# Optimization experiments

Hardware: AMD Instinct MI355X
Metric: run time of the kernel (lower is better)

Reference implementation:

```python
import jax, jax.numpy as jnp
import numpy as np

FEATURE_DIM = 128

def setup_inputs() -> dict:
    key0 = jax.random.key(0)
    k1, k2, k3 = jax.random.split(key0, 3)
    B, NQ, NK, D = 4, 4096, 4096, FEATURE_DIM
    return {
        "target": jax.random.normal(k1, (B, NQ, D), dtype=jnp.float32),
        "key": jax.random.normal(k2, (B, NK, D), dtype=jnp.float32),
        "value": jax.random.normal(k3, (B, NK, D), dtype=jnp.float32),
    }

def reference(target, key, value):
    # Lan_K F: scores = target @ key^T / sqrt(d); weights = softmax(scores); out = weights @ value
    scale = 1.0 / np.sqrt(FEATURE_DIM).astype(np.float32)
    scores = jnp.einsum('bqd,bkd->bqk', target, key) * scale  # [B, NQ, NK]
    weights = jax.nn.softmax(scores, axis=-1)
    return jnp.einsum('bqk,bkd->bqd', weights, value)  # [B, NQ, D]
```

## Files before the change

### kernel.cpp

```cpp
#include <hip/hip_runtime.h>
#include <stdint.h>

#define B_ 4
#define NQ_ 4096
#define NK_ 4096
#define D_ 128
#define BM_ 64
#define BN_ 128
#define NITER_ (NK_/BN_)
#define PS_ 136
#define OS_ 66

typedef __attribute__((ext_vector_type(8))) short short8;
typedef __attribute__((ext_vector_type(4))) float floatx4;
typedef unsigned int u32;

union frag_u { u32 u[4]; short8 s; };
union pair_u { u32 u[2]; uint2 v; };

__device__ __forceinline__ unsigned short f2bf_rne(float x){
  union { float f; u32 u; } c; c.f = x;
  u32 u = c.u;
  return (unsigned short)((u + 0x7fffu + ((u >> 16) & 1u)) >> 16);
}
__device__ __forceinline__ u32 pk2bf(float a, float b){
  union { float f; u32 u; } x, y; x.f = a; y.f = b;
  return ((x.u + 0x8000u) >> 16) | ((y.u + 0x8000u) & 0xffff0000u);
}

__global__ __launch_bounds__(256) void prep_kernel(
    const float* __restrict__ k, const float* __restrict__ v,
    unsigned short* __restrict__ kf, unsigned short* __restrict__ vf){
  __shared__ __align__(16) char smem[40960];
  const int t = threadIdx.x;
  const int blk = blockIdx.x;
  if (blk < 128){
    int b = blk >> 5, it = blk & 31;
    const float* src = k + ((size_t)b*NK_ + it*BN_)*D_;
    #pragma unroll
    for (int i = 0; i < 16; i++){
      int f = t + i*256;
      int row = f >> 5, c4 = f & 31;
      float4 a = *(const float4*)(src + (size_t)row*D_ + c4*4);
      ushort4 s;
      s.x = f2bf_rne(a.x); s.y = f2bf_rne(a.y);
      s.z = f2bf_rne(a.z); s.w = f2bf_rne(a.w);
      int kg = row >> 5, rem = row & 31;
      int dh = (rem >> 2) & 1;
      int l15 = ((rem >> 3) << 2) | (rem & 3);
      int wq = kg*2 + dh;
      int j = c4 >> 3, l4 = (c4 >> 1) & 3, half = c4 & 1;
      *(ushort4*)(smem + (wq*4 + j)*1088 + l4*272 + l15*16 + half*8) = s;
    }
    __syncthreads();
    unsigned short* dst = kf + (size_t)(b*32 + it)*2048*8;
    #pragma unroll
    for (int i = 0; i < 8; i++){
      int c = t + i*256;
      int lane = c & 63, j = (c >> 6) & 3, wq = c >> 8;
      int l15 = lane & 15, l4 = lane >> 4;
      short8 x = *(const short8*)(smem + (wq*4 + j)*1088 + l4*272 + l15*16);
      *(short8*)(dst + (size_t)c*8) = x;
    }
  } else {
    int blk2 = blk - 128;
    int b = blk2 >> 5, it = blk2 & 31;
    const float* src = v + ((size_t)b*NK_ + it*BN_)*D_;
    #pragma unroll
    for (int i = 0; i < 16; i++){
      int f = t + i*256;
      int row = f >> 5, c4 = f & 31;
      float4 a = *(const float4*)(src + (size_t)row*D_ + c4*4);
      float vals[4] = {a.x, a.y, a.z, a.w};
      int kk = row & 7, l4a = (row >> 3) & 3, kga = row >> 5;
      #pragma unroll
      for (int jj = 0; jj < 4; jj++){
        int d = c4*4 + jj;
        int dh = d >> 6, dt = (d >> 4) & 3, l15 = d & 15;
        int c = ((kga*2 + dh)*4 + dt)*64 + l4a*16 + l15;
        *(unsigned short*)(smem + c*16 + (c>>2)*16 + kk*2) = f2bf_rne(vals[jj]);
      }
    }
    __syncthreads();
    unsigned short* dst = vf + (size_t)(b*32 + it)*2048*8;
    #pragma unroll
    for (int i = 0; i < 8; i++){
      int c = t + i*256;
      short8 x = *(const short8*)(smem + c*16 + (c>>2)*16);
      *(short8*)(dst + (size_t)c*8) = x;
    }
  }
}

__global__ __launch_bounds__(512, 2) void attn_kernel(
    const float* __restrict__ Qf, const unsigned short* __restrict__ Kb,
    const unsigned short* __restrict__ Vt, float* __restrict__ Out){
  __shared__ __align__(16) char sm[69632];
  unsigned short* smP = (unsigned short*)sm;
  float* smO = (float*)sm;
  float* smL = (float*)(sm + 67584);

  const int bi = blockIdx.x;
  const int b  = (bi >> 1) & 3;
  const int qt = ((bi >> 3) << 1) | (bi & 1);
  const int q0 = qt * BM_;
  const int tid = threadIdx.x;
  const int w = tid >> 6, lane = tid & 63;
  const int kg = w >> 1, dh = w & 1;
  const int l15 = lane & 15, l4 = lane >> 4;

  const short8* Kfrag = (const short8*)Kb;
  const short8* Vfrag = (const short8*)Vt;
  const size_t FSTRIDE = 8*4*64;
  const size_t fbase = (((size_t)b*32)*8 + w)*4*64 + lane;

  short8 qf[4][4];
  {
    const float* qp = Qf + ((size_t)b*NQ_ + q0)*D_;
    #pragma unroll
    for (int nb = 0; nb < 4; nb++)
      #pragma unroll
      for (int kb = 0; kb < 4; kb++){
        const float* p = qp + (size_t)(nb*16 + l15)*D_ + kb*32 + l4*8;
        float4 a = *(const float4*)p;
        float4 c4 = *(const float4*)(p + 4);
        frag_u f;
        f.u[0] = pk2bf(a.x, a.y);  f.u[1] = pk2bf(a.z, a.w);
        f.u[2] = pk2bf(c4.x, c4.y); f.u[3] = pk2bf(c4.z, c4.w);
        qf[nb][kb] = f.s;
      }
  }

  short8 kfA[4], kfB[4], vfA[4], vfB[4];
  #pragma unroll
  for (int j = 0; j < 4; j++) kfA[j] = Kfrag[fbase + j*64];
  #pragma unroll
  for (int dt = 0; dt < 4; dt++) vfA[dt] = Vfrag[fbase + dt*64];
  #pragma unroll
  for (int j = 0; j < 4; j++) kfB[j] = Kfrag[fbase + FSTRIDE + j*64];
  #pragma unroll
  for (int dt = 0; dt < 4; dt++) vfB[dt] = Vfrag[fbase + FSTRIDE + dt*64];

  floatx4 o[4][4];
  #pragma unroll
  for (int nb = 0; nb < 4; nb++)
    #pragma unroll
    for (int dt = 0; dt < 4; dt++) o[nb][dt] = (floatx4)0.0f;
  float lsum[4] = {0.f, 0.f, 0.f, 0.f};

  const float SL = 0.08838834764831845f * 1.4426950408889634f;
  const size_t prow = (size_t)kg*32 + l4*8;

  for (int it = 0; it < NITER_; it += 2){
    {
      floatx4 s[4];
      #pragma unroll
      for (int nb = 0; nb < 4; nb++){
        s[nb] = (floatx4)0.0f;
        s[nb] = __builtin_amdgcn_mfma_f32_16x16x32_bf16(kfA[0], qf[nb][0], s[nb], 0,0,0);
        s[nb] = __builtin_amdgcn_mfma_f32_16x16x32_bf16(kfA[1], qf[nb][1], s[nb], 0,0,0);
        s[nb] = __builtin_amdgcn_mfma_f32_16x16x32_bf16(kfA[2], qf[nb][2], s[nb], 0,0,0);
        s[nb] = __builtin_amdgcn_mfma_f32_16x16x32_bf16(kfA[3], qf[nb][3], s[nb], 0,0,0);
      }
      if (it + 2 < NITER_){
        #pragma unroll
        for (int j = 0; j < 4; j++)
          kfA[j] = Kfrag[fbase + (size_t)(it+2)*FSTRIDE + j*64];
      }
      unsigned short* smPb = smP;
      #pragma unroll
      for (int nb = 0; nb < 4; nb++){
        float p0 = __builtin_amdgcn_exp2f(s[nb][0] * SL);
        float p1 = __builtin_amdgcn_exp2f(s[nb][1] * SL);
        float p2 = __builtin_amdgcn_exp2f(s[nb][2] * SL);
        float p3 = __builtin_amdgcn_exp2f(s[nb][3] * SL);
        lsum[nb] += (p0 + p1) + (p2 + p3);
        pair_u pp; pp.u[0] = pk2bf(p0, p1); pp.u[1] = pk2bf(p2, p3);
        *(uint2*)(smPb + (size_t)(nb*16 + l15)*PS_ + prow + dh*4) = pp.v;
      }
      asm volatile("s_waitcnt lgkmcnt(0)" ::: "memory");
      __builtin_amdgcn_s_barrier();
      asm volatile("" ::: "memory");
      short8 pf[4];
      #pragma unroll
      for (int nb = 0; nb < 4; nb++)
        pf[nb] = *(const short8*)(smPb + (size_t)(nb*16 + l15)*PS_ + prow);
      #pragma unroll
      for (int nb = 0; nb < 4; nb++)
        #pragma unroll
        for (int dt = 0; dt < 4; dt++)
          o[nb][dt] = __builtin_amdgcn_mfma_f32_16x16x32_bf16(pf[nb], vfA[dt], o[nb][dt], 0,0,0);
      if (it + 2 < NITER_){
        #pragma unroll
        for (int dt = 0; dt < 4; dt++)
          vfA[dt] = Vfrag[fbase + (size_t)(it+2)*FSTRIDE + dt*64];
      }
    }
    {
      floatx4 s[4];
      #pragma unroll
      for (int nb = 0; nb < 4; nb++){
        s[nb] = (floatx4)0.0f;
        s[nb] = __builtin_amdgcn_mfma_f32_16x16x32_bf16(kfB[0], qf[nb][0], s[nb], 0,0,0);
        s[nb] = __builtin_amdgcn_mfma_f32_16x16x32_bf16(kfB[1], qf[nb][1], s[nb], 0,0,0);
        s[nb] = __builtin_amdgcn_mfma_f32_16x16x32_bf16(kfB[2], qf[nb][2], s[nb], 0,0,0);
        s[nb] = __builtin_amdgcn_mfma_f32_16x16x32_bf16(kfB[3], qf[nb][3], s[nb], 0,0,0);
      }
      if (it + 3 < NITER_){
        #pragma unroll
        for (int j = 0; j < 4; j++)
          kfB[j] = Kfrag[fbase + (size_t)(it+3)*FSTRIDE + j*64];
      }
      unsigned short* smPb = smP + 64*PS_;
      #pragma unroll
      for (int nb = 0; nb < 4; nb++){
        float p0 = __builtin_amdgcn_exp2f(s[nb][0] * SL);
        float p1 = __builtin_amdgcn_exp2f(s[nb][1] * SL);
        float p2 = __builtin_amdgcn_exp2f(s[nb][2] * SL);
        float p3 = __builtin_amdgcn_exp2f(s[nb][3] * SL);
        lsum[nb] += (p0 + p1) + (p2 + p3);
        pair_u pp; pp.u[0] = pk2bf(p0, p1); pp.u[1] = pk2bf(p2, p3);
        *(uint2*)(smPb + (size_t)(nb*16 + l15)*PS_ + prow + dh*4) = pp.v;
      }
      asm volatile("s_waitcnt lgkmcnt(0)" ::: "memory");
      __builtin_amdgcn_s_barrier();
      asm volatile("" ::: "memory");
      short8 pf[4];
      #pragma unroll
      for (int nb = 0; nb < 4; nb++)
        pf[nb] = *(const short8*)(smPb + (size_t)(nb*16 + l15)*PS_ + prow);
      #pragma unroll
      for (int nb = 0; nb < 4; nb++)
        #pragma unroll
        for (int dt = 0; dt < 4; dt++)
          o[nb][dt] = __builtin_amdgcn_mfma_f32_16x16x32_bf16(pf[nb], vfB[dt], o[nb][dt], 0,0,0);
      if (it + 3 < NITER_){
        #pragma unroll
        for (int dt = 0; dt < 4; dt++)
          vfB[dt] = Vfrag[fbase + (size_t)(it+3)*FSTRIDE + dt*64];
      }
    }
  }

  #pragma unroll
  for (int nb = 0; nb < 4; nb++){
    float v = lsum[nb];
    v += __shfl_xor(v, 16);
    v += __shfl_xor(v, 32);
    lsum[nb] = v;
  }
  if (l4 == 0)
    #pragma unroll
    for (int nb = 0; nb < 4; nb++)
      smL[w*64 + nb*16 + l15] = lsum[nb];

  __syncthreads();

  if (w >= 4){
    float* r = smO + (size_t)(w - 4) * 4224;
    #pragma unroll
    for (int nb = 0; nb < 4; nb++)
      #pragma unroll
      for (int dt = 0; dt < 4; dt++)
        #pragma unroll
        for (int q = 0; q < 4; q++)
          r[(size_t)(nb*16 + l4*4 + q)*OS_ + dt*16 + l15] = o[nb][dt][q];
  }
  __syncthreads();
  if (w < 4){
    float* r = smO + (size_t)w * 4224;
    #pragma unroll
    for (int nb = 0; nb < 4; nb++)
      #pragma unroll
      for (int dt = 0; dt < 4; dt++)
        #pragma unroll
        for (int q = 0; q < 4; q++)
          o[nb][dt][q] += r[(size_t)(nb*16 + l4*4 + q)*OS_ + dt*16 + l15];
  }
  __syncthreads();
  if (w == 2 || w == 3){
    float* r = smO + (size_t)(w - 2) * 4224;
    #pragma unroll
    for (int nb = 0; nb < 4; nb++)
      #pragma unroll
      for (int dt = 0; dt < 4; dt++)
        #pragma unroll
        for (int q = 0; q < 4; q++)
          r[(size_t)(nb*16 + l4*4 + q)*OS_ + dt*16 + l15] = o[nb][dt][q];
  }
  __syncthreads();
  if (w < 2){
    float* r = smO + (size_t)w * 4224;
    float* og = Out + ((size_t)b*NQ_ + q0)*D_ + dh*64;
    #pragma unroll
    for (int nb = 0; nb < 4; nb++)
      #pragma unroll
      for (int q = 0; q < 4; q++){
        int row = nb*16 + l4*4 + q;
        float lt = 0.f;
        #pragma unroll
        for (int w2 = 0; w2 < 8; w2++) lt += smL[w2*64 + row];
        float inv = 1.0f / lt;
        #pragma unroll
        for (int dt = 0; dt < 4; dt++){
          float val = o[nb][dt][q] + r[(size_t)row*OS_ + dt*16 + l15];
          og[(size_t)row*D_ + dt*16 + l15] = val * inv;
        }
      }
  }
}

extern "C" void kernel_launch(void* const* d_in, const int* in_sizes, int n_in,
                              void* d_out, int out_size, void* d_ws, size_t ws_size,
                              hipStream_t stream){
  const float* q = (const float*)d_in[0];
  const float* k = (const float*)d_in[1];
  const float* v = (const float*)d_in[2];
  float* out = (float*)d_out;
  unsigned short* kb = (unsigned short*)d_ws;
  unsigned short* vt = kb + (size_t)B_*NK_*D_;
  prep_kernel<<<256, 256, 0, stream>>>(k, v, kb, vt);
  attn_kernel<<<256, 512, 0, stream>>>(q, kb, vt, out);
}
```

Baseline: 117.3 us.

## Fuse K/V prep and attention into one kernel with grid barriers

Merges the bf16 K/V repacking kernel into the attention kernel, separated by a software grid barrier built on a global atomic counter. The repacked K/V now live in the output buffer rather than the workspace, and a second grid barrier keeps every block from writing its output until all blocks have finished reading the fragments. The aim is to remove one kernel launch and the gap between the two kernels. The barrier relies on all 256 blocks being resident at the same time, and the output buffer holds exactly as many bytes as the two bf16 copies, so no space is left over.

```diff
diff --git a/kernel.cpp b/kernel.cpp
--- a/kernel.cpp
+++ b/kernel.cpp
@@ -28,18 +28,38 @@
   return ((x.u + 0x8000u) >> 16) | ((y.u + 0x8000u) & 0xffff0000u);
 }
 
-__global__ __launch_bounds__(256) void prep_kernel(
-    const float* __restrict__ k, const float* __restrict__ v,
-    unsigned short* __restrict__ kf, unsigned short* __restrict__ vf){
-  __shared__ __align__(16) char smem[40960];
-  const int t = threadIdx.x;
-  const int blk = blockIdx.x;
-  if (blk < 128){
-    int b = blk >> 5, it = blk & 31;
-    const float* src = k + ((size_t)b*NK_ + it*BN_)*D_;
-    #pragma unroll
-    for (int i = 0; i < 16; i++){
-      int f = t + i*256;
+__device__ unsigned g_bar = 0;
+__device__ __forceinline__ void grid_barrier(){
+  __threadfence();
+  __syncthreads();
+  if (threadIdx.x == 0){
+    unsigned old = __hip_atomic_fetch_add(&g_bar, 1u, __ATOMIC_ACQ_REL,
+                                          __HIP_MEMORY_SCOPE_AGENT);
+    unsigned target = (old & ~255u) + 256u;
+    while ((int)(__hip_atomic_load(&g_bar, __ATOMIC_ACQUIRE,
+                                   __HIP_MEMORY_SCOPE_AGENT) - target) < 0)
+      __builtin_amdgcn_s_sleep(8);
+  }
+  __syncthreads();
+  __threadfence();
+}
+
+__global__ __launch_bounds__(512, 2) void fused_kernel(
+    const float* __restrict__ Qf, const float* __restrict__ Kin,
+    const float* __restrict__ Vin, float* Out){
+  __shared__ __align__(16) char sm[69632];
+  const int tid = threadIdx.x;
+  const int bi = blockIdx.x;
+
+  unsigned short* kb = (unsigned short*)Out;
+  unsigned short* vt = kb + (size_t)B_*NK_*D_;
+
+  if (bi < 128){
+    int b = bi >> 5, it = bi & 31;
+    const float* src = Kin + ((size_t)b*NK_ + it*BN_)*D_;
+    #pragma unroll
+    for (int i = 0; i < 8; i++){
+      int f = tid + i*512;
       int row = f >> 5, c4 = f & 31;
       float4 a = *(const float4*)(src + (size_t)row*D_ + c4*4);
       ushort4 s;
@@ -50,25 +70,25 @@
       int l15 = ((rem >> 3) << 2) | (rem & 3);
       int wq = kg*2 + dh;
       int j = c4 >> 3, l4 = (c4 >> 1) & 3, half = c4 & 1;
-      *(ushort4*)(smem + (wq*4 + j)*1088 + l4*272 + l15*16 + half*8) = s;
+      *(ushort4*)(sm + (wq*4 + j)*1088 + l4*272 + l15*16 + half*8) = s;
     }
     __syncthreads();
-    unsigned short* dst = kf + (size_t)(b*32 + it)*2048*8;
-    #pragma unroll
-    for (int i = 0; i < 8; i++){
-      int c = t + i*256;
+    unsigned short* dst = kb + (size_t)(b*32 + it)*2048*8;
+    #pragma unroll
+    for (int i = 0; i < 4; i++){
+      int c = tid + i*512;
       int lane = c & 63, j = (c >> 6) & 3, wq = c >> 8;
       int l15 = lane & 15, l4 = lane >> 4;
-      short8 x = *(const short8*)(smem + (wq*4 + j)*1088 + l4*272 + l15*16);
+      short8 x = *(const short8*)(sm + (wq*4 + j)*1088 + l4*272 + l15*16);
       *(short8*)(dst + (size_t)c*8) = x;
     }
   } else {
-    int blk2 = blk - 128;
+    int blk2 = bi - 128;
     int b = blk2 >> 5, it = blk2 & 31;
-    const float* src = v + ((size_t)b*NK_ + it*BN_)*D_;
-    #pragma unroll
-    for (int i = 0; i < 16; i++){
-      int f = t + i*256;
+    const float* src = Vin + ((size_t)b*NK_ + it*BN_)*D_;
+    #pragma unroll
+    for (int i = 0; i < 8; i++){
+      int f = tid + i*512;
       int row = f >> 5, c4 = f & 31;
       float4 a = *(const float4*)(src + (size_t)row*D_ + c4*4);
       float vals[4] = {a.x, a.y, a.z, a.w};
@@ -78,39 +98,34 @@
         int d = c4*4 + jj;
         int dh = d >> 6, dt = (d >> 4) & 3, l15 = d & 15;
         int c = ((kga*2 + dh)*4 + dt)*64 + l4a*16 + l15;
-        *(unsigned short*)(smem + c*16 + (c>>2)*16 + kk*2) = f2bf_rne(vals[jj]);
+        *(unsigned short*)(sm + c*16 + (c>>2)*16 + kk*2) = f2bf_rne(vals[jj]);
       }
     }
     __syncthreads();
-    unsigned short* dst = vf + (size_t)(b*32 + it)*2048*8;
-    #pragma unroll
-    for (int i = 0; i < 8; i++){
-      int c = t + i*256;
-      short8 x = *(const short8*)(smem + c*16 + (c>>2)*16);
+    unsigned short* dst = vt + (size_t)(b*32 + it)*2048*8;
+    #pragma unroll
+    for (int i = 0; i < 4; i++){
+      int c = tid + i*512;
+      short8 x = *(const short8*)(sm + c*16 + (c>>2)*16);
       *(short8*)(dst + (size_t)c*8) = x;
     }
   }
-}
-
-__global__ __launch_bounds__(512, 2) void attn_kernel(
-    const float* __restrict__ Qf, const unsigned short* __restrict__ Kb,
-    const unsigned short* __restrict__ Vt, float* __restrict__ Out){
-  __shared__ __align__(16) char sm[69632];
+
+  grid_barrier();
+
   unsigned short* smP = (unsigned short*)sm;
   float* smO = (float*)sm;
   float* smL = (float*)(sm + 67584);
 
-  const int bi = blockIdx.x;
   const int b  = (bi >> 1) & 3;
   const int qt = ((bi >> 3) << 1) | (bi & 1);
   const int q0 = qt * BM_;
-  const int tid = threadIdx.x;
   const int w = tid >> 6, lane = tid & 63;
   const int kg = w >> 1, dh = w & 1;
   const int l15 = lane & 15, l4 = lane >> 4;
 
-  const short8* Kfrag = (const short8*)Kb;
-  const short8* Vfrag = (const short8*)Vt;
+  const short8* Kfrag = (const short8*)kb;
+  const short8* Vfrag = (const short8*)vt;
   const size_t FSTRIDE = 8*4*64;
   const size_t fbase = (((size_t)b*32)*8 + w)*4*64 + lane;
 
@@ -120,14 +135,14 @@
     #pragma unroll
     for (int nb = 0; nb < 4; nb++)
       #pragma unroll
-      for (int kb = 0; kb < 4; kb++){
-        const float* p = qp + (size_t)(nb*16 + l15)*D_ + kb*32 + l4*8;
+      for (int kbq = 0; kbq < 4; kbq++){
+        const float* p = qp + (size_t)(nb*16 + l15)*D_ + kbq*32 + l4*8;
         float4 a = *(const float4*)p;
         float4 c4 = *(const float4*)(p + 4);
         frag_u f;
         f.u[0] = pk2bf(a.x, a.y);  f.u[1] = pk2bf(a.z, a.w);
         f.u[2] = pk2bf(c4.x, c4.y); f.u[3] = pk2bf(c4.z, c4.w);
-        qf[nb][kb] = f.s;
+        qf[nb][kbq] = f.s;
       }
   }
 
@@ -242,6 +257,8 @@
     }
   }
 
+  grid_barrier();
+
   #pragma unroll
   for (int nb = 0; nb < 4; nb++){
     float v = lsum[nb];
@@ -317,8 +334,6 @@
   const float* k = (const float*)d_in[1];
   const float* v = (const float*)d_in[2];
   float* out = (float*)d_out;
-  unsigned short* kb = (unsigned short*)d_ws;
-  unsigned short* vt = kb + (size_t)B_*NK_*D_;
-  prep_kernel<<<256, 256, 0, stream>>>(k, v, kb, vt);
-  attn_kernel<<<256, 512, 0, stream>>>(q, kb, vt, out);
-}
+  (void)d_ws; (void)ws_size;
+  fused_kernel<<<256, 512, 0, stream>>>(q, k, v, out);
+}
```

After: 291.6 us. 149% more time.

## Compute scores redundantly per wave pair to drop LDS P exchange and barriers

Applied to the files above, without the earlier changes.

Each wave now computes the QK^T scores for the full 32-key slice it consumes in the PV product, using two sets of K fragments. The exponentiated probabilities are packed straight into the MFMA A-operand register fragment instead of going through shared memory. This removes the per-subiteration LDS write/read and the workgroup barrier. In exchange the QK MFMA work is doubled, since both dh waves compute the same scores, and K fragment register pressure grows. The row-sum normalisation is halved (2/lt) because lsum is now counted twice.

```diff
diff --git a/kernel.cpp b/kernel.cpp
--- a/kernel.cpp
+++ b/kernel.cpp
@@ -8,7 +8,6 @@
 #define BM_ 64
 #define BN_ 128
 #define NITER_ (NK_/BN_)
-#define PS_ 136
 #define OS_ 66
 
 typedef __attribute__((ext_vector_type(8))) short short8;
@@ -16,7 +15,6 @@
 typedef unsigned int u32;
 
 union frag_u { u32 u[4]; short8 s; };
-union pair_u { u32 u[2]; uint2 v; };
 
 __device__ __forceinline__ unsigned short f2bf_rne(float x){
   union { float f; u32 u; } c; c.f = x;
@@ -92,11 +90,51 @@
   }
 }
 
+#define SUBITER(KF, VF, ITN) do {                                              \
+  _Pragma("unroll")                                                            \
+  for (int nb = 0; nb < 4; nb++){                                              \
+    floatx4 s0 = (floatx4)0.0f, s1 = (floatx4)0.0f;                            \
+    s0 = __builtin_amdgcn_mfma_f32_16x16x32_bf16(KF[0][0], qf[nb][0], s0,0,0,0);\
+    s0 = __builtin_amdgcn_mfma_f32_16x16x32_bf16(KF[0][1], qf[nb][1], s0,0,0,0);\
+    s0 = __builtin_amdgcn_mfma_f32_16x16x32_bf16(KF[0][2], qf[nb][2], s0,0,0,0);\
+    s0 = __builtin_amdgcn_mfma_f32_16x16x32_bf16(KF[0][3], qf[nb][3], s0,0,0,0);\
+    s1 = __builtin_amdgcn_mfma_f32_16x16x32_bf16(KF[1][0], qf[nb][0], s1,0,0,0);\
+    s1 = __builtin_amdgcn_mfma_f32_16x16x32_bf16(KF[1][1], qf[nb][1], s1,0,0,0);\
+    s1 = __builtin_amdgcn_mfma_f32_16x16x32_bf16(KF[1][2], qf[nb][2], s1,0,0,0);\
+    s1 = __builtin_amdgcn_mfma_f32_16x16x32_bf16(KF[1][3], qf[nb][3], s1,0,0,0);\
+    float p0 = __builtin_amdgcn_exp2f(s0[0] * SL);                             \
+    float p1 = __builtin_amdgcn_exp2f(s0[1] * SL);                             \
+    float p2 = __builtin_amdgcn_exp2f(s0[2] * SL);                             \
+    float p3 = __builtin_amdgcn_exp2f(s0[3] * SL);                             \
+    float p4 = __builtin_amdgcn_exp2f(s1[0] * SL);                             \
+    float p5 = __builtin_amdgcn_exp2f(s1[1] * SL);                             \
+    float p6 = __builtin_amdgcn_exp2f(s1[2] * SL);                             \
+    float p7 = __builtin_amdgcn_exp2f(s1[3] * SL);                             \
+    lsum[nb] += ((p0 + p1) + (p2 + p3)) + ((p4 + p5) + (p6 + p7));             \
+    frag_u pf;                                                                 \
+    pf.u[0] = pk2bf(p0, p1); pf.u[1] = pk2bf(p2, p3);                          \
+    pf.u[2] = pk2bf(p4, p5); pf.u[3] = pk2bf(p6, p7);                          \
+    o[nb][0] = __builtin_amdgcn_mfma_f32_16x16x32_bf16(pf.s, VF[0], o[nb][0],0,0,0);\
+    o[nb][1] = __builtin_amdgcn_mfma_f32_16x16x32_bf16(pf.s, VF[1], o[nb][1],0,0,0);\
+    o[nb][2] = __builtin_amdgcn_mfma_f32_16x16x32_bf16(pf.s, VF[2], o[nb][2],0,0,0);\
+    o[nb][3] = __builtin_amdgcn_mfma_f32_16x16x32_bf16(pf.s, VF[3], o[nb][3],0,0,0);\
+  }                                                                            \
+  if ((ITN) < NITER_){                                                         \
+    _Pragma("unroll")                                                          \
+    for (int h = 0; h < 2; h++)                                                \
+      _Pragma("unroll")                                                        \
+      for (int j = 0; j < 4; j++)                                              \
+        KF[h][j] = Kfrag[kbase[h] + (size_t)(ITN)*FSTRIDE + j*64];             \
+    _Pragma("unroll")                                                          \
+    for (int dt = 0; dt < 4; dt++)                                             \
+      VF[dt] = Vfrag[vbase + (size_t)(ITN)*FSTRIDE + dt*64];                   \
+  }                                                                            \
+} while(0)
+
 __global__ __launch_bounds__(512, 2) void attn_kernel(
     const float* __restrict__ Qf, const unsigned short* __restrict__ Kb,
     const unsigned short* __restrict__ Vt, float* __restrict__ Out){
   __shared__ __align__(16) char sm[69632];
-  unsigned short* smP = (unsigned short*)sm;
   float* smO = (float*)sm;
   float* smL = (float*)(sm + 67584);
 
@@ -112,7 +150,10 @@
   const short8* Kfrag = (const short8*)Kb;
   const short8* Vfrag = (const short8*)Vt;
   const size_t FSTRIDE = 8*4*64;
-  const size_t fbase = (((size_t)b*32)*8 + w)*4*64 + lane;
+  size_t kbase[2];
+  kbase[0] = ((size_t)b*256 + kg*2 + 0)*256 + lane;
+  kbase[1] = ((size_t)b*256 + kg*2 + 1)*256 + lane;
+  const size_t vbase = ((size_t)b*256 + w)*256 + lane;
 
   short8 qf[4][4];
   {
@@ -120,26 +161,30 @@
     #pragma unroll
     for (int nb = 0; nb < 4; nb++)
       #pragma unroll
-      for (int kb = 0; kb < 4; kb++){
-        const float* p = qp + (size_t)(nb*16 + l15)*D_ + kb*32 + l4*8;
+      for (int kbq = 0; kbq < 4; kbq++){
+        const float* p = qp + (size_t)(nb*16 + l15)*D_ + kbq*32 + l4*8;
         float4 a = *(const float4*)p;
         float4 c4 = *(const float4*)(p + 4);
         frag_u f;
         f.u[0] = pk2bf(a.x, a.y);  f.u[1] = pk2bf(a.z, a.w);
         f.u[2] = pk2bf(c4.x, c4.y); f.u[3] = pk2bf(c4.z, c4.w);
-        qf[nb][kb] = f.s;
+        qf[nb][kbq] = f.s;
       }
   }
 
-  short8 kfA[4], kfB[4], vfA[4], vfB[4];
-  #pragma unroll
-  for (int j = 0; j < 4; j++) kfA[j] = Kfrag[fbase + j*64];
-  #pragma unroll
-  for (int dt = 0; dt < 4; dt++) vfA[dt] = Vfrag[fbase + dt*64];
-  #pragma unroll
-  for (int j = 0; j < 4; j++) kfB[j] = Kfrag[fbase + FSTRIDE + j*64];
-  #pragma unroll
-  for (int dt = 0; dt < 4; dt++) vfB[dt] = Vfrag[fbase + FSTRIDE + dt*64];
+  short8 kfE[2][4], kfO[2][4], vfE[4], vfO[4];
+  #pragma unroll
+  for (int h = 0; h < 2; h++)
+    #pragma unroll
+    for (int j = 0; j < 4; j++){
+      kfE[h][j] = Kfrag[kbase[h] + j*64];
+      kfO[h][j] = Kfrag[kbase[h] + FSTRIDE + j*64];
+    }
+  #pragma unroll
+  for (int dt = 0; dt < 4; dt++){
+    vfE[dt] = Vfrag[vbase + dt*64];
+    vfO[dt] = Vfrag[vbase + FSTRIDE + dt*64];
+  }
 
   floatx4 o[4][4];
   #pragma unroll
@@ -149,97 +194,10 @@
   float lsum[4] = {0.f, 0.f, 0.f, 0.f};
 
   const float SL = 0.08838834764831845f * 1.4426950408889634f;
-  const size_t prow = (size_t)kg*32 + l4*8;
 
   for (int it = 0; it < NITER_; it += 2){
-    {
-      floatx4 s[4];
-      #pragma unroll
-      for (int nb = 0; nb < 4; nb++){
-        s[nb] = (floatx4)0.0f;
-        s[nb] = __builtin_amdgcn_mfma_f32_16x16x32_bf16(kfA[0], qf[nb][0], s[nb], 0,0,0);
-        s[nb] = __builtin_amdgcn_mfma_f32_16x16x32_bf16(kfA[1], qf[nb][1], s[nb], 0,0,0);
-        s[nb] = __builtin_amdgcn_mfma_f32_16x16x32_bf16(kfA[2], qf[nb][2], s[nb], 0,0,0);
-        s[nb] = __builtin_amdgcn_mfma_f32_16x16x32_bf16(kfA[3], qf[nb][3], s[nb], 0,0,0);
-      }
-      if (it + 2 < NITER_){
-        #pragma unroll
-        for (int j = 0; j < 4; j++)
-          kfA[j] = Kfrag[fbase + (size_t)(it+2)*FSTRIDE + j*64];
-      }
-      unsigned short* smPb = smP;
-      #pragma unroll
-      for (int nb = 0; nb < 4; nb++){
-        float p0 = __builtin_amdgcn_exp2f(s[nb][0] * SL);
-        float p1 = __builtin_amdgcn_exp2f(s[nb][1] * SL);
-        float p2 = __builtin_amdgcn_exp2f(s[nb][2] * SL);
-        float p3 = __builtin_amdgcn_exp2f(s[nb][3] * SL);
-        lsum[nb] += (p0 + p1) + (p2 + p3);
-        pair_u pp; pp.u[0] = pk2bf(p0, p1); pp.u[1] = pk2bf(p2, p3);
-        *(uint2*)(smPb + (size_t)(nb*16 + l15)*PS_ + prow + dh*4) = pp.v;
-      }
-      asm volatile("s_waitcnt lgkmcnt(0)" ::: "memory");
-      __builtin_amdgcn_s_barrier();
-      asm volatile("" ::: "memory");
-      short8 pf[4];
-      #pragma unroll
-      for (int nb = 0; nb < 4; nb++)
-        pf[nb] = *(const short8*)(smPb + (size_t)(nb*16 + l15)*PS_ + prow);
-      #pragma unroll
-      for (int nb = 0; nb < 4; nb++)
-        #pragma unroll
-        for (int dt = 0; dt < 4; dt++)
-          o[nb][dt] = __builtin_amdgcn_mfma_f32_16x16x32_bf16(pf[nb], vfA[dt], o[nb][dt], 0,0,0);
-      if (it + 2 < NITER_){
-        #pragma unroll
-        for (int dt = 0; dt < 4; dt++)
-          vfA[dt] = Vfrag[fbase + (size_t)(it+2)*FSTRIDE + dt*64];
-      }
-    }
-    {
-      floatx4 s[4];
-      #pragma unroll
-      for (int nb = 0; nb < 4; nb++){
-        s[nb] = (floatx4)0.0f;
-        s[nb] = __builtin_amdgcn_mfma_f32_16x16x32_bf16(kfB[0], qf[nb][0], s[nb], 0,0,0);
-        s[nb] = __builtin_amdgcn_mfma_f32_16x16x32_bf16(kfB[1], qf[nb][1], s[nb], 0,0,0);
-        s[nb] = __builtin_amdgcn_mfma_f32_16x16x32_bf16(kfB[2], qf[nb][2], s[nb], 0,0,0);
-        s[nb] = __builtin_amdgcn_mfma_f32_16x16x32_bf16(kfB[3], qf[nb][3], s[nb], 0,0,0);
-      }
-      if (it + 3 < NITER_){
-        #pragma unroll
-        for (int j = 0; j < 4; j++)
-          kfB[j] = Kfrag[fbase + (size_t)(it+3)*FSTRIDE + j*64];
-      }
-      unsigned short* smPb = smP + 64*PS_;
-      #pragma unroll
-      for (int nb = 0; nb < 4; nb++){
-        float p0 = __builtin_amdgcn_exp2f(s[nb][0] * SL);
-        float p1 = __builtin_amdgcn_exp2f(s[nb][1] * SL);
-        float p2 = __builtin_amdgcn_exp2f(s[nb][2] * SL);
-        float p3 = __builtin_amdgcn_exp2f(s[nb][3] * SL);
-        lsum[nb] += (p0 + p1) + (p2 + p3);
-        pair_u pp; pp.u[0] = pk2bf(p0, p1); pp.u[1] = pk2bf(p2, p3);
-        *(uint2*)(smPb + (size_t)(nb*16 + l15)*PS_ + prow + dh*4) = pp.v;
-      }
-      asm volatile("s_waitcnt lgkmcnt(0)" ::: "memory");
-      __builtin_amdgcn_s_barrier();
-      asm volatile("" ::: "memory");
-      short8 pf[4];
-      #pragma unroll
-      for (int nb = 0; nb < 4; nb++)
-        pf[nb] = *(const short8*)(smPb + (size_t)(nb*16 + l15)*PS_ + prow);
-      #pragma unroll
-      for (int nb = 0; nb < 4; nb++)
-        #pragma unroll
-        for (int dt = 0; dt < 4; dt++)
-          o[nb][dt] = __builtin_amdgcn_mfma_f32_16x16x32_bf16(pf[nb], vfB[dt], o[nb][dt], 0,0,0);
-      if (it + 3 < NITER_){
-        #pragma unroll
-        for (int dt = 0; dt < 4; dt++)
-          vfB[dt] = Vfrag[fbase + (size_t)(it+3)*FSTRIDE + dt*64];
-      }
-    }
+    SUBITER(kfE, vfE, it + 2);
+    SUBITER(kfO, vfO, it + 3);
   }
 
   #pragma unroll
@@ -300,7 +258,7 @@
         float lt = 0.f;
         #pragma unroll
         for (int w2 = 0; w2 < 8; w2++) lt += smL[w2*64 + row];
-        float inv = 1.0f / lt;
+        float inv = 2.0f / lt;
         #pragma unroll
         for (int dt = 0; dt < 4; dt++){
           float val = o[nb][dt][q] + r[(size_t)row*OS_ + dt*16 + l15];
```

Measured after the change: 234.9 us. 100% more time.
